# Kernel optimization log

Hardware: AMD Instinct MI355X
Metric: run time of the kernel (lower is better)

The kernel has to match this reference:

```python
import jax, jax.numpy as jnp
import numpy as np

EPS = 1e-5          # InstanceNorm2d default eps
SLOPE = 0.01        # LeakyReLU default negative_slope
C = 256


def setup_inputs() -> dict:
    key = jax.random.key(0)
    k = jax.random.split(key, 5)
    B, H, W = 8, 128, 128
    x = jax.random.normal(k[0], (B, C, H, W), dtype=jnp.float32)
    # attn: Conv2d(C, C//4, 1, bias=False) then Conv2d(C//4, C, 1, bias=False)
    attn_w1 = jax.random.normal(k[1], (C // 4, C), dtype=jnp.float32) * (1.0 / np.sqrt(C))
    attn_w2 = jax.random.normal(k[2], (C, C // 4), dtype=jnp.float32) * (1.0 / np.sqrt(C // 4))
    # refine: depthwise Conv2d(C, C, 3, padding=1, groups=C) with bias
    refine_w = jax.random.normal(k[3], (C, 1, 3, 3), dtype=jnp.float32) * (1.0 / 3.0)
    refine_b = jax.random.normal(k[4], (C,), dtype=jnp.float32) * 0.01
    return {"x": x, "attn_w1": attn_w1, "attn_w2": attn_w2,
            "refine_w": refine_w, "refine_b": refine_b}


def reference(x, attn_w1, attn_w2, refine_w, refine_b):
    # The torch module runs pywt wavedec2 -> waverec2 on x[b,c].detach().
    # With db2 (symmetric mode) and H,W divisible by 2^level, waverec2 is a
    # perfect-reconstruction identity and interpolate to (H,W) is a no-op,
    # so x_wave == stop_gradient(x) exactly.
    xw = jax.lax.stop_gradient(x)

    # --- channel attention (squeeze-excite with 1x1 convs == GEMMs) ---
    p = jnp.mean(xw, axis=(2, 3))                      # [B, C] global avg pool
    h = jax.nn.leaky_relu(p @ attn_w1.T, SLOPE)        # [B, C//4]
    a = jax.nn.sigmoid(h @ attn_w2.T)                  # [B, C]
    y = xw * a[:, :, None, None]

    # --- depthwise 3x3 refine conv ---
    y = jax.lax.conv_general_dilated(
        y, refine_w, window_strides=(1, 1), padding='SAME',
        feature_group_count=C,
        dimension_numbers=('NCHW', 'OIHW', 'NCHW'))
    y = y + refine_b[None, :, None, None]

    # --- InstanceNorm2d (affine=False, biased variance) ---
    mu = jnp.mean(y, axis=(2, 3), keepdims=True)
    var = jnp.mean(jnp.square(y - mu), axis=(2, 3), keepdims=True)
    y = (y - mu) * jax.lax.rsqrt(var + EPS)

    return jax.nn.leaky_relu(y, SLOPE)
```

## Files before the change

kernel.cpp:

```cpp
#include <hip/hip_runtime.h>
#include <hip/hip_bf16.h>
#include <math.h>

#define NPLANE 2048
#define HW     16384
#define WW     128
#define SLOPE  0.01f
#define EPS    1e-5f

__global__ __launch_bounds__(256) void k_plane_mean(const float* __restrict__ x,
                                                    float* __restrict__ p) {
    const int plane = blockIdx.x;
    const float4* x4 = (const float4*)(x + (size_t)plane * HW);
    float s = 0.f;
#pragma unroll
    for (int i = 0; i < 16; ++i) {
        float4 v = x4[i * 256 + threadIdx.x];
        s += (v.x + v.y) + (v.z + v.w);
    }
#pragma unroll
    for (int off = 32; off; off >>= 1) s += __shfl_down(s, off, 64);
    __shared__ float red[4];
    const int wave = threadIdx.x >> 6, lane = threadIdx.x & 63;
    if (lane == 0) red[wave] = s;
    __syncthreads();
    if (threadIdx.x == 0) {
        float t = (red[0] + red[1]) + (red[2] + red[3]);
        p[plane] = t * (1.f / (float)HW);
    }
}

__global__ __launch_bounds__(256) void k_main(const float* __restrict__ x,
                                              const float* __restrict__ w1,
                                              const float* __restrict__ w2,
                                              const float* __restrict__ rw,
                                              const float* __restrict__ p,
                                              float* __restrict__ out) {
    __shared__ float hs[64];
    __shared__ float red[8];
    __shared__ float sh_a;

    const int plane = blockIdx.x;
    const int b = plane >> 8;
    const int ch = plane & 255;

    {
        const int j = threadIdx.x >> 2;
        const int part = threadIdx.x & 3;
        const float4* pr = (const float4*)(p + b * 256 + part * 64);
        const float4* wr = (const float4*)(w1 + j * 256 + part * 64);
        float acc = 0.f;
#pragma unroll
        for (int k = 0; k < 16; ++k) {
            float4 pv = pr[k], wv = wr[k];
            acc += pv.x * wv.x + pv.y * wv.y + pv.z * wv.z + pv.w * wv.w;
        }
        acc += __shfl_xor(acc, 1, 64);
        acc += __shfl_xor(acc, 2, 64);
        if (part == 0) hs[j] = acc > 0.f ? acc : SLOPE * acc;
    }
    __syncthreads();
    if (threadIdx.x < 64) {
        float v = w2[ch * 64 + threadIdx.x] * hs[threadIdx.x];
#pragma unroll
        for (int off = 32; off; off >>= 1) v += __shfl_down(v, off, 64);
        if (threadIdx.x == 0) sh_a = 1.f / (1.f + expf(-v));
    }

    const float w_0 = rw[ch * 9 + 0], w_1 = rw[ch * 9 + 1], w_2 = rw[ch * 9 + 2];
    const float w_3 = rw[ch * 9 + 3], w_4 = rw[ch * 9 + 4], w_5 = rw[ch * 9 + 5];
    const float w_6 = rw[ch * 9 + 6], w_7 = rw[ch * 9 + 7], w_8 = rw[ch * 9 + 8];

    const float* xp = x + (size_t)plane * HW;
    const int c = threadIdx.x & 127;
    const int r0 = (threadIdx.x >> 7) * 64;

#define LOADROW(row, L, M, Q)                                          \
    do {                                                               \
        const int _r = (row);                                          \
        if (_r >= 0 && _r <= 127) {                                    \
            const float* rp = xp + _r * WW;                            \
            M = rp[c];                                                 \
            L = (c > 0)   ? rp[c - 1] : 0.f;                           \
            Q = (c < 127) ? rp[c + 1] : 0.f;                           \
        } else { L = 0.f; M = 0.f; Q = 0.f; }                          \
    } while (0)

#define CONV9() (w_0 * l0 + w_1 * m0 + w_2 * q0                        \
               + w_3 * l1 + w_4 * m1 + w_5 * q1                        \
               + w_6 * l2 + w_7 * m2 + w_8 * q2)

    float l0, m0, q0, l1, m1, q1, l2, m2, q2;
    LOADROW(r0 - 1, l0, m0, q0);
    LOADROW(r0,     l1, m1, q1);
    float s = 0.f, sq = 0.f;
#pragma unroll 8
    for (int j = 0; j < 64; ++j) {
        LOADROW(r0 + j + 1, l2, m2, q2);
        const float conv = CONV9();
        s += conv;
        sq += conv * conv;
        l0 = l1; m0 = m1; q0 = q1;
        l1 = l2; m1 = m2; q1 = q2;
    }

#pragma unroll
    for (int off = 32; off; off >>= 1) {
        s  += __shfl_down(s,  off, 64);
        sq += __shfl_down(sq, off, 64);
    }
    const int wave = threadIdx.x >> 6, lane = threadIdx.x & 63;
    if (lane == 0) { red[wave] = s; red[4 + wave] = sq; }
    __syncthreads();
    const float S  = (red[0] + red[1]) + (red[2] + red[3]);
    const float SQ = (red[4] + red[5]) + (red[6] + red[7]);
    const float mean_c = S * (1.f / (float)HW);
    const float var_c  = SQ * (1.f / (float)HW) - mean_c * mean_c;
    const float a      = sh_a;
    const float scale  = a * rsqrtf(a * a * var_c + EPS);

    float* op = out + (size_t)plane * HW;
    LOADROW(r0 - 1, l0, m0, q0);
    LOADROW(r0,     l1, m1, q1);
#pragma unroll 8
    for (int j = 0; j < 64; ++j) {
        LOADROW(r0 + j + 1, l2, m2, q2);
        const float conv = CONV9();
        float v = scale * (conv - mean_c);
        v = v > 0.f ? v : SLOPE * v;
        op[(r0 + j) * WW + c] = v;
        l0 = l1; m0 = m1; q0 = q1;
        l1 = l2; m1 = m2; q1 = q2;
    }
#undef LOADROW
#undef CONV9
}

extern "C" void kernel_launch(void* const* d_in, const int* in_sizes, int n_in,
                              void* d_out, int out_size, void* d_ws, size_t ws_size,
                              hipStream_t stream) {
    const float* x  = (const float*)d_in[0];
    const float* w1 = (const float*)d_in[1];
    const float* w2 = (const float*)d_in[2];
    const float* rw = (const float*)d_in[3];
    float* out = (float*)d_out;

    float* p = (float*)d_ws;

    k_plane_mean<<<NPLANE, 256, 0, stream>>>(x, p);
    k_main<<<NPLANE, 256, 0, stream>>>(x, w1, w2, rw, p, out);
}
```

Before: 307.7 us.

## Move conv statistics into first pass and vectorize depthwise conv with float4 shuffles

The first kernel now computes the plane mean together with the unscaled conv sum and sum of squares, so the output kernel reads x once instead of twice. This relies on the attention scale factoring out of the conv, with its effect on the variance applied analytically. Both kernels load float4 rows and fetch the left and right halo through lane shuffles instead of three scalar loads per pixel. Output uses nontemporal vector stores, and launch bounds ask for 8 blocks per CU. The first pass now performs the full conv arithmetic.

```diff
diff --git a/kernel.cpp b/kernel.cpp
--- a/kernel.cpp
+++ b/kernel.cpp
@@ -8,52 +8,108 @@
 #define SLOPE  0.01f
 #define EPS    1e-5f
 
-__global__ __launch_bounds__(256) void k_plane_mean(const float* __restrict__ x,
-                                                    float* __restrict__ p) {
+typedef float v4f __attribute__((ext_vector_type(4)));
+
+__device__ __forceinline__ void load_row(const float* __restrict__ xp, int r,
+                                         int c4, int lane32,
+                                         float4& m, float& L, float& R) {
+    int rc = r;
+    if (rc < 0) rc = 0;
+    if (rc > 127) rc = 127;
+    const float va = (r == rc) ? 1.f : 0.f;
+    float4 v = *(const float4*)(xp + rc * WW + c4);
+    m.x = v.x * va; m.y = v.y * va; m.z = v.z * va; m.w = v.w * va;
+    L = __shfl_up(m.w, 1, 64);
+    if (lane32 == 0) L = 0.f;
+    R = __shfl_down(m.x, 1, 64);
+    if (lane32 == 31) R = 0.f;
+}
+
+#define CONV4(o0, o1, o2, o3)                                                \
+    float o0 = w_0*L0   + w_1*m0.x + w_2*m0.y                                \
+             + w_3*L1   + w_4*m1.x + w_5*m1.y                                \
+             + w_6*L2   + w_7*m2.x + w_8*m2.y;                               \
+    float o1 = w_0*m0.x + w_1*m0.y + w_2*m0.z                                \
+             + w_3*m1.x + w_4*m1.y + w_5*m1.z                                \
+             + w_6*m2.x + w_7*m2.y + w_8*m2.z;                               \
+    float o2 = w_0*m0.y + w_1*m0.z + w_2*m0.w                                \
+             + w_3*m1.y + w_4*m1.z + w_5*m1.w                                \
+             + w_6*m2.y + w_7*m2.z + w_8*m2.w;                               \
+    float o3 = w_0*m0.z + w_1*m0.w + w_2*R0                                  \
+             + w_3*m1.z + w_4*m1.w + w_5*R1                                  \
+             + w_6*m2.z + w_7*m2.w + w_8*R2
+
+#define SLIDE() do { m0 = m1; L0 = L1; R0 = R1; m1 = m2; L1 = L2; R1 = R2; } while (0)
+
+__global__ __launch_bounds__(256, 8) void k_stats(const float* __restrict__ x,
+                                                  const float* __restrict__ rw,
+                                                  float* __restrict__ p,
+                                                  float* __restrict__ cstats) {
     const int plane = blockIdx.x;
-    const float4* x4 = (const float4*)(x + (size_t)plane * HW);
-    float s = 0.f;
+    const int ch = plane & 255;
+    const float* xp = x + (size_t)plane * HW;
+    const int lane32 = threadIdx.x & 31;
+    const int c4 = lane32 * 4;
+    const int r0 = (threadIdx.x >> 5) * 16;
+
+    const float w_0 = rw[ch*9+0], w_1 = rw[ch*9+1], w_2 = rw[ch*9+2];
+    const float w_3 = rw[ch*9+3], w_4 = rw[ch*9+4], w_5 = rw[ch*9+5];
+    const float w_6 = rw[ch*9+6], w_7 = rw[ch*9+7], w_8 = rw[ch*9+8];
+
+    float4 m0, m1, m2;
+    float L0, R0, L1, R1, L2, R2;
+    load_row(xp, r0 - 1, c4, lane32, m0, L0, R0);
+    load_row(xp, r0,     c4, lane32, m1, L1, R1);
+
+    float xs = 0.f, s = 0.f, sq = 0.f;
+#pragma unroll 4
+    for (int j = 0; j < 16; ++j) {
+        load_row(xp, r0 + j + 1, c4, lane32, m2, L2, R2);
+        CONV4(o0, o1, o2, o3);
+        s  += (o0 + o1) + (o2 + o3);
+        sq += o0*o0 + o1*o1 + o2*o2 + o3*o3;
+        xs += (m1.x + m1.y) + (m1.z + m1.w);
+        SLIDE();
+    }
+
 #pragma unroll
-    for (int i = 0; i < 16; ++i) {
-        float4 v = x4[i * 256 + threadIdx.x];
-        s += (v.x + v.y) + (v.z + v.w);
+    for (int off = 32; off; off >>= 1) {
+        xs += __shfl_down(xs, off, 64);
+        s  += __shfl_down(s,  off, 64);
+        sq += __shfl_down(sq, off, 64);
     }
-#pragma unroll
-    for (int off = 32; off; off >>= 1) s += __shfl_down(s, off, 64);
-    __shared__ float red[4];
+    __shared__ float red[12];
     const int wave = threadIdx.x >> 6, lane = threadIdx.x & 63;
-    if (lane == 0) red[wave] = s;
+    if (lane == 0) { red[wave] = xs; red[4+wave] = s; red[8+wave] = sq; }
     __syncthreads();
     if (threadIdx.x == 0) {
-        float t = (red[0] + red[1]) + (red[2] + red[3]);
-        p[plane] = t * (1.f / (float)HW);
+        p[plane]            = ((red[0]+red[1]) + (red[2]+red[3])) * (1.f/(float)HW);
+        cstats[plane*2]     = (red[4]+red[5]) + (red[6]+red[7]);
+        cstats[plane*2 + 1] = (red[8]+red[9]) + (red[10]+red[11]);
     }
 }
 
-__global__ __launch_bounds__(256) void k_main(const float* __restrict__ x,
-                                              const float* __restrict__ w1,
-                                              const float* __restrict__ w2,
-                                              const float* __restrict__ rw,
-                                              const float* __restrict__ p,
-                                              float* __restrict__ out) {
+__global__ __launch_bounds__(256, 8) void k_out(const float* __restrict__ x,
+                                                const float* __restrict__ w1,
+                                                const float* __restrict__ w2,
+                                                const float* __restrict__ rw,
+                                                const float* __restrict__ p,
+                                                const float* __restrict__ cstats,
+                                                float* __restrict__ out) {
     __shared__ float hs[64];
-    __shared__ float red[8];
-    __shared__ float sh_a;
-
+    __shared__ float sh_mean, sh_scale;
     const int plane = blockIdx.x;
-    const int b = plane >> 8;
-    const int ch = plane & 255;
+    const int b = plane >> 8, ch = plane & 255;
 
     {
-        const int j = threadIdx.x >> 2;
-        const int part = threadIdx.x & 3;
-        const float4* pr = (const float4*)(p + b * 256 + part * 64);
+        const int j = threadIdx.x >> 2, part = threadIdx.x & 3;
+        const float4* pr = (const float4*)(p  + b * 256 + part * 64);
         const float4* wr = (const float4*)(w1 + j * 256 + part * 64);
         float acc = 0.f;
 #pragma unroll
         for (int k = 0; k < 16; ++k) {
             float4 pv = pr[k], wv = wr[k];
-            acc += pv.x * wv.x + pv.y * wv.y + pv.z * wv.z + pv.w * wv.w;
+            acc += pv.x*wv.x + pv.y*wv.y + pv.z*wv.z + pv.w*wv.w;
         }
         acc += __shfl_xor(acc, 1, 64);
         acc += __shfl_xor(acc, 2, 64);
@@ -64,76 +120,45 @@
         float v = w2[ch * 64 + threadIdx.x] * hs[threadIdx.x];
 #pragma unroll
         for (int off = 32; off; off >>= 1) v += __shfl_down(v, off, 64);
-        if (threadIdx.x == 0) sh_a = 1.f / (1.f + expf(-v));
+        if (threadIdx.x == 0) {
+            const float a  = 1.f / (1.f + expf(-v));
+            const float mc = cstats[plane*2] * (1.f/(float)HW);
+            const float vc = cstats[plane*2 + 1] * (1.f/(float)HW) - mc * mc;
+            sh_mean  = mc;
+            sh_scale = a * rsqrtf(a * a * vc + EPS);
+        }
     }
 
-    const float w_0 = rw[ch * 9 + 0], w_1 = rw[ch * 9 + 1], w_2 = rw[ch * 9 + 2];
-    const float w_3 = rw[ch * 9 + 3], w_4 = rw[ch * 9 + 4], w_5 = rw[ch * 9 + 5];
-    const float w_6 = rw[ch * 9 + 6], w_7 = rw[ch * 9 + 7], w_8 = rw[ch * 9 + 8];
+    const float w_0 = rw[ch*9+0], w_1 = rw[ch*9+1], w_2 = rw[ch*9+2];
+    const float w_3 = rw[ch*9+3], w_4 = rw[ch*9+4], w_5 = rw[ch*9+5];
+    const float w_6 = rw[ch*9+6], w_7 = rw[ch*9+7], w_8 = rw[ch*9+8];
+
+    __syncthreads();
+    const float mean_c = sh_mean, scale = sh_scale;
 
     const float* xp = x + (size_t)plane * HW;
-    const int c = threadIdx.x & 127;
-    const int r0 = (threadIdx.x >> 7) * 64;
+    float* op = out + (size_t)plane * HW;
+    const int lane32 = threadIdx.x & 31;
+    const int c4 = lane32 * 4;
+    const int r0 = (threadIdx.x >> 5) * 16;
 
-#define LOADROW(row, L, M, Q)                                          \
-    do {                                                               \
-        const int _r = (row);                                          \
-        if (_r >= 0 && _r <= 127) {                                    \
-            const float* rp = xp + _r * WW;                            \
-            M = rp[c];                                                 \
-            L = (c > 0)   ? rp[c - 1] : 0.f;                           \
-            Q = (c < 127) ? rp[c + 1] : 0.f;                           \
-        } else { L = 0.f; M = 0.f; Q = 0.f; }                          \
-    } while (0)
+    float4 m0, m1, m2;
+    float L0, R0, L1, R1, L2, R2;
+    load_row(xp, r0 - 1, c4, lane32, m0, L0, R0);
+    load_row(xp, r0,     c4, lane32, m1, L1, R1);
 
-#define CONV9() (w_0 * l0 + w_1 * m0 + w_2 * q0                        \
-               + w_3 * l1 + w_4 * m1 + w_5 * q1                        \
-               + w_6 * l2 + w_7 * m2 + w_8 * q2)
-
-    float l0, m0, q0, l1, m1, q1, l2, m2, q2;
-    LOADROW(r0 - 1, l0, m0, q0);
-    LOADROW(r0,     l1, m1, q1);
-    float s = 0.f, sq = 0.f;
-#pragma unroll 8
-    for (int j = 0; j < 64; ++j) {
-        LOADROW(r0 + j + 1, l2, m2, q2);
-        const float conv = CONV9();
-        s += conv;
-        sq += conv * conv;
-        l0 = l1; m0 = m1; q0 = q1;
-        l1 = l2; m1 = m2; q1 = q2;
+#pragma unroll 4
+    for (int j = 0; j < 16; ++j) {
+        load_row(xp, r0 + j + 1, c4, lane32, m2, L2, R2);
+        CONV4(o0, o1, o2, o3);
+        v4f res;
+        float t0 = scale * (o0 - mean_c); res.x = t0 > 0.f ? t0 : SLOPE * t0;
+        float t1 = scale * (o1 - mean_c); res.y = t1 > 0.f ? t1 : SLOPE * t1;
+        float t2 = scale * (o2 - mean_c); res.z = t2 > 0.f ? t2 : SLOPE * t2;
+        float t3 = scale * (o3 - mean_c); res.w = t3 > 0.f ? t3 : SLOPE * t3;
+        __builtin_nontemporal_store(res, (v4f*)(op + (r0 + j) * WW + c4));
+        SLIDE();
     }
-
-#pragma unroll
-    for (int off = 32; off; off >>= 1) {
-        s  += __shfl_down(s,  off, 64);
-        sq += __shfl_down(sq, off, 64);
-    }
-    const int wave = threadIdx.x >> 6, lane = threadIdx.x & 63;
-    if (lane == 0) { red[wave] = s; red[4 + wave] = sq; }
-    __syncthreads();
-    const float S  = (red[0] + red[1]) + (red[2] + red[3]);
-    const float SQ = (red[4] + red[5]) + (red[6] + red[7]);
-    const float mean_c = S * (1.f / (float)HW);
-    const float var_c  = SQ * (1.f / (float)HW) - mean_c * mean_c;
-    const float a      = sh_a;
-    const float scale  = a * rsqrtf(a * a * var_c + EPS);
-
-    float* op = out + (size_t)plane * HW;
-    LOADROW(r0 - 1, l0, m0, q0);
-    LOADROW(r0,     l1, m1, q1);
-#pragma unroll 8
-    for (int j = 0; j < 64; ++j) {
-        LOADROW(r0 + j + 1, l2, m2, q2);
-        const float conv = CONV9();
-        float v = scale * (conv - mean_c);
-        v = v > 0.f ? v : SLOPE * v;
-        op[(r0 + j) * WW + c] = v;
-        l0 = l1; m0 = m1; q0 = q1;
-        l1 = l2; m1 = m2; q1 = q2;
-    }
-#undef LOADROW
-#undef CONV9
 }
 
 extern "C" void kernel_launch(void* const* d_in, const int* in_sizes, int n_in,
@@ -145,8 +170,9 @@
     const float* rw = (const float*)d_in[3];
     float* out = (float*)d_out;
 
-    float* p = (float*)d_ws;
+    float* p      = (float*)d_ws;
+    float* cstats = p + NPLANE;
 
-    k_plane_mean<<<NPLANE, 256, 0, stream>>>(x, p);
-    k_main<<<NPLANE, 256, 0, stream>>>(x, w1, w2, rw, p, out);
+    k_stats<<<NPLANE, 256, 0, stream>>>(x, rw, p, cstats);
+    k_out  <<<NPLANE, 256, 0, stream>>>(x, w1, w2, rw, p, cstats, out);
 }
```

Result: faster. 274.8 us (-10.7%).
